# Performance work log

Measured on AMD Instinct MI355X. Metric: run time of the kernel, lower is better.

Reference implementation:

```python
import jax, jax.numpy as jnp
import numpy as np

N_NODES = 20000
N_EDGES = 160000
N_GRAPHS = 500
F_IN = 128
HID = 512
N_CLS = 10
N_LAYERS = 3
BN_EPS = 1e-5
BN_BIAS = 1e-4  # BatchNorm1d weight init to 1, bias to 0.0001


def bn(x):
    # training-mode BatchNorm1d with gamma=1, beta=1e-4 (per module init)
    m = jnp.mean(x, axis=0)
    v = jnp.mean((x - m) ** 2, axis=0)
    return (x - m) * jax.lax.rsqrt(v + BN_EPS) + BN_BIAS


def gcn_norm(row, col, edge_weight, num_nodes):
    # add self loops with weight 1, symmetric deg^-1/2 normalization
    loop = jnp.arange(num_nodes)
    r = jnp.concatenate([row, loop])
    c = jnp.concatenate([col, loop])
    w = jnp.concatenate([edge_weight, jnp.ones((num_nodes,), edge_weight.dtype)])
    deg = jax.ops.segment_sum(w, r, num_segments=num_nodes)
    dis = jnp.where(deg > 0, jax.lax.rsqrt(deg), jnp.zeros_like(deg))
    return r, c, dis[r] * w * dis[c]


def gcn(x, W, b, r, c, norm):
    # x@W then gather source feats, scale by norm, scatter-add to targets
    h = x @ W
    out = jax.ops.segment_sum(norm[:, None] * h[c], r, num_segments=x.shape[0])
    return out + b


def readout(x, W1, b1, W2, b2):
    x = bn(x) @ W1 + b1
    x = jax.nn.relu(x)
    x = bn(x) @ W2 + b2
    return jax.nn.log_softmax(x, axis=-1)


def setup_inputs() -> dict:
    key = jax.random.key(0)
    ks = iter(jax.random.split(key, 40))

    def lin(k, fin, fout):
        return jax.random.normal(k, (fin, fout), jnp.float32) * (1.0 / np.sqrt(fin))

    x = jax.random.normal(next(ks), (N_NODES, F_IN), jnp.float32)
    edge_index = jax.random.randint(next(ks), (2, N_EDGES), 0, N_NODES)
    batch = jnp.sort(jax.random.randint(next(ks), (N_NODES,), 0, N_GRAPHS))
    perm = jax.random.permutation(next(ks), N_GRAPHS)

    inp = {"x": x, "edge_index": edge_index, "batch": batch, "perm": perm}
    inp["conv_feat_W"] = lin(next(ks), F_IN, HID)
    inp["conv_feat_b"] = jnp.zeros((HID,), jnp.float32)
    inp["convs_W"] = jax.random.normal(next(ks), (N_LAYERS, HID, HID), jnp.float32) * (1.0 / np.sqrt(HID))
    inp["convs_b"] = jnp.zeros((N_LAYERS, HID), jnp.float32)
    inp["edge_att_W"] = lin(next(ks), 2 * HID, 2)
    inp["edge_att_b"] = jnp.zeros((2,), jnp.float32)
    inp["node_att_W"] = lin(next(ks), HID, 2)
    inp["node_att_b"] = jnp.zeros((2,), jnp.float32)
    inp["ctx_W"] = lin(next(ks), HID, HID)
    inp["ctx_b"] = jnp.zeros((HID,), jnp.float32)
    inp["obj_W"] = lin(next(ks), HID, HID)
    inp["obj_b"] = jnp.zeros((HID,), jnp.float32)
    for tag in ("c", "o", "co"):
        inp[f"fc1_{tag}_W"] = lin(next(ks), HID, HID)
        inp[f"fc1_{tag}_b"] = jnp.zeros((HID,), jnp.float32)
        inp[f"fc2_{tag}_W"] = lin(next(ks), HID, N_CLS)
        inp[f"fc2_{tag}_b"] = jnp.zeros((N_CLS,), jnp.float32)
    return inp


def reference(x, edge_index, batch, perm,
              conv_feat_W, conv_feat_b, convs_W, convs_b,
              edge_att_W, edge_att_b, node_att_W, node_att_b,
              ctx_W, ctx_b, obj_W, obj_b,
              fc1_c_W, fc1_c_b, fc2_c_W, fc2_c_b,
              fc1_o_W, fc1_o_b, fc2_o_W, fc2_o_b,
              fc1_co_W, fc1_co_b, fc2_co_W, fc2_co_b):
    row, col = edge_index[0], edge_index[1]
    n = x.shape[0]

    x = bn(x)
    x = jax.nn.relu(x @ conv_feat_W + conv_feat_b)  # conv_feat has gfn=True: pure linear

    # unweighted symmetric norm, shared by all stacked convs
    r1, c1, nrm1 = gcn_norm(row, col, jnp.ones((row.shape[0],), x.dtype), n)
    for i in range(N_LAYERS):
        x = bn(x)
        x = jax.nn.relu(gcn(x, convs_W[i], convs_b[i], r1, c1, nrm1))

    edge_rep = jnp.concatenate([x[row], x[col]], axis=-1)        # [E, 2H]
    edge_att = jax.nn.softmax(edge_rep @ edge_att_W + edge_att_b, axis=-1)
    node_att = jax.nn.softmax(x @ node_att_W + node_att_b, axis=-1)

    xc = node_att[:, :1] * x
    xo = node_att[:, 1:] * x

    rc, cc, nc = gcn_norm(row, col, edge_att[:, 0], n)
    ro, co_, no_ = gcn_norm(row, col, edge_att[:, 1], n)
    xc = jax.nn.relu(gcn(bn(xc), ctx_W, ctx_b, rc, cc, nc))
    xo = jax.nn.relu(gcn(bn(xo), obj_W, obj_b, ro, co_, no_))

    xc = jax.ops.segment_sum(xc, batch, num_segments=N_GRAPHS)   # global_add_pool
    xo = jax.ops.segment_sum(xo, batch, num_segments=N_GRAPHS)

    xc_logis = readout(xc, fc1_c_W, fc1_c_b, fc2_c_W, fc2_c_b)
    xo_logis = readout(xo, fc1_o_W, fc1_o_b, fc2_o_W, fc2_o_b)
    # cat_or_add == 'add', with_random shuffle realized by perm
    xco_logis = readout(xc[perm] + xo, fc1_co_W, fc1_co_b, fc2_co_W, fc2_co_b)
    return xc_logis, xo_logis, xco_logis
```

## Files before the change

kernel.cpp:

```cpp
#include <hip/hip_runtime.h>
#include <stdint.h>

#define NN 20000
#define NE 160000
#define NG 500
#define FIN 128
#define HID 512
#define NCLS 10
#define BNG 256
#define NB3 32

typedef __attribute__((ext_vector_type(8))) short short8;
typedef __attribute__((ext_vector_type(4))) float f32x4;
typedef __attribute__((ext_vector_type(4))) unsigned short ushort4v;

__device__ __forceinline__ float bf2f(unsigned int u){
  union{unsigned int i; float f;} x; x.i = u<<16; return x.f;
}
__device__ __forceinline__ unsigned short f2bf(float f){
  union{float f; unsigned int i;} x; x.f=f;
  unsigned int r = x.i + 0x7fffu + ((x.i>>16)&1u);
  return (unsigned short)(r>>16);
}
__device__ __forceinline__ unsigned int pk2(float a, float b){
  return (unsigned int)f2bf(a) | ((unsigned int)f2bf(b) << 16);
}

__device__ __forceinline__ void gload16(unsigned short* lds, const unsigned short* g){
  __builtin_amdgcn_global_load_lds((const __attribute__((address_space(1))) unsigned int*)g,
                                   (__attribute__((address_space(3))) unsigned int*)lds,
                                   16, 0, 0);
}

__device__ __forceinline__ void fma8(float* acc, uint4 v, float w){
  acc[0] += w*bf2f(v.x & 0xffffu); acc[1] += w*bf2f(v.x >> 16);
  acc[2] += w*bf2f(v.y & 0xffffu); acc[3] += w*bf2f(v.y >> 16);
  acc[4] += w*bf2f(v.z & 0xffffu); acc[5] += w*bf2f(v.z >> 16);
  acc[6] += w*bf2f(v.w & 0xffffu); acc[7] += w*bf2f(v.w >> 16);
}

__global__ void sentinel_k(float* out){ out[0] = 12345.0f; }

struct W2BT { const float* src[9]; unsigned short* dst[9]; };
__global__ void setup_all(W2BT p, int* __restrict__ cnt, int* __restrict__ fillc,
                          float* __restrict__ degc, float* __restrict__ dego,
                          float* __restrict__ Sc, float* __restrict__ So,
                          float* __restrict__ stats6){
  int idx = blockIdx.x*blockDim.x + threadIdx.x;
  if (idx < FIN*HID + 8*HID*HID){
    int seg, off, K;
    if (idx < FIN*HID){ seg = 0; off = idx; K = FIN; }
    else {
      int r = idx - FIN*HID;
      seg = 1 + (r >> 18); off = r & (HID*HID-1); K = HID;
    }
    int k = off >> 9, n = off & 511;
    p.dst[seg][(size_t)n*K + k] = f2bf(p.src[seg][off]);
  }
  if (idx < NN){ cnt[idx]=0; fillc[idx]=0; degc[idx]=1.0f; dego[idx]=1.0f; Sc[idx]=0.f; So[idx]=0.f; }
  if (idx < 6*1024) stats6[idx] = 0.f;
}

__global__ __launch_bounds__(1024) void bnstats_p(const float* __restrict__ X, int M, int F,
                                                  float* __restrict__ partials){
  __shared__ float lds[1024*9];
  const int t = threadIdx.x;
  const int cg = F >> 2;
  const int cid = t & (cg-1);
  const int rid = t / cg;
  const int rpb = 1024 / cg;
  float s0=0,s1=0,s2=0,s3=0,q0=0,q1=0,q2=0,q3=0;
  const int rowsPer = (M + BNG - 1)/BNG;
  int r0 = blockIdx.x*rowsPer, r1 = r0 + rowsPer; if (r1 > M) r1 = M;
  for (int r = r0 + rid; r < r1; r += rpb){
    float4 v = *(const float4*)&X[(size_t)r*F + cid*4];
    s0+=v.x; q0+=v.x*v.x; s1+=v.y; q1+=v.y*v.y; s2+=v.z; q2+=v.z*v.z; s3+=v.w; q3+=v.w*v.w;
  }
  int base = (rid*cg + cid)*9;
  lds[base+0]=s0; lds[base+1]=s1; lds[base+2]=s2; lds[base+3]=s3;
  lds[base+4]=q0; lds[base+5]=q1; lds[base+6]=q2; lds[base+7]=q3;
  __syncthreads();
  if (t < cg*8){
    int ci = t >> 3, i = t & 7;
    float acc = 0.f;
    for (int g=0; g<rpb; ++g) acc += lds[(g*cg + ci)*9 + i];
    int col = ci*4 + (i & 3);
    partials[(size_t)blockIdx.x*(2*F) + ((i < 4) ? col : F + col)] = acc;
  }
}

__global__ __launch_bounds__(1024) void bnstats_dual(const unsigned short* __restrict__ X,
                                                     const float* __restrict__ na,
                                                     float* __restrict__ partials){
  __shared__ float lds[1024*17];
  const int t = threadIdx.x;
  const int cid = t & 127;
  const int rid = t >> 7;
  float sC[4]={0,0,0,0}, qC[4]={0,0,0,0}, sO[4]={0,0,0,0}, qO[4]={0,0,0,0};
  const int rowsPer = (NN + BNG - 1)/BNG;
  int r0 = blockIdx.x*rowsPer, r1 = r0 + rowsPer; if (r1 > NN) r1 = NN;
  for (int r = r0 + rid; r < r1; r += 8){
    float a0 = na[2*r], a1 = na[2*r+1];
    uint2 u = *(const uint2*)&X[(size_t)r*HID + cid*4];
    float e[4] = {bf2f(u.x & 0xffffu), bf2f(u.x >> 16), bf2f(u.y & 0xffffu), bf2f(u.y >> 16)};
#pragma unroll
    for (int i=0;i<4;i++){
      float vc = e[i]*a0, vo = e[i]*a1;
      sC[i]+=vc; qC[i]+=vc*vc; sO[i]+=vo; qO[i]+=vo*vo;
    }
  }
  int base = (rid*128 + cid)*17;
#pragma unroll
  for (int i=0;i<4;i++){
    lds[base+i]=sC[i]; lds[base+4+i]=qC[i]; lds[base+8+i]=sO[i]; lds[base+12+i]=qO[i];
  }
  __syncthreads();
  for (int idx = t; idx < 2048; idx += 1024){
    int ci = idx >> 4, i = idx & 15;
    float acc = 0.f;
    for (int g=0; g<8; ++g) acc += lds[(g*128 + ci)*17 + i];
    int grp = i >> 2, col = ci*4 + (i & 3);
    partials[(size_t)blockIdx.x*2048 + grp*HID + col] = acc;
  }
}

__global__ void bnfin_red(const float* __restrict__ partials, int stride, int off,
                          int M, int F, float* __restrict__ mstat){
  __shared__ float lds[4][64][2];
  int t = threadIdx.x;
  int cl = t & 63, ch = t >> 6;
  int c = blockIdx.x*64 + cl;
  float s = 0.f, q = 0.f;
  if (c < F){
    for (int b = ch*64; b < ch*64 + 64; ++b){
      s += partials[(size_t)b*stride + off + c];
      q += partials[(size_t)b*stride + off + F + c];
    }
  }
  lds[ch][cl][0] = s; lds[ch][cl][1] = q;
  __syncthreads();
  if (ch == 0 && c < F){
    s = lds[0][cl][0]+lds[1][cl][0]+lds[2][cl][0]+lds[3][cl][0];
    q = lds[0][cl][1]+lds[1][cl][1]+lds[2][cl][1]+lds[3][cl][1];
    float m = s/(float)M;
    float v = q/(float)M - m*m;
    mstat[c] = m;
    mstat[F+c] = rsqrtf(v + 1e-5f);
  }
}

__global__ void bnfin_red2(const float* __restrict__ partials, float* __restrict__ mstatCO){
  __shared__ float lds[4][64][2];
  int t = threadIdx.x;
  int cl = t & 63, ch = t >> 6;
  int c = blockIdx.x*64 + cl;
  int off = blockIdx.y*1024;
  float s = 0.f, q = 0.f;
  for (int b = ch*64; b < ch*64 + 64; ++b){
    s += partials[(size_t)b*2048 + off + c];
    q += partials[(size_t)b*2048 + off + HID + c];
  }
  lds[ch][cl][0] = s; lds[ch][cl][1] = q;
  __syncthreads();
  if (ch == 0){
    s = lds[0][cl][0]+lds[1][cl][0]+lds[2][cl][0]+lds[3][cl][0];
    q = lds[0][cl][1]+lds[1][cl][1]+lds[2][cl][1]+lds[3][cl][1];
    float m = s/(float)NN;
    float v = q/(float)NN - m*m;
    mstatCO[blockIdx.y*1024 + c] = m;
    mstatCO[blockIdx.y*1024 + HID + c] = rsqrtf(v + 1e-5f);
  }
}

__global__ void bncast(const float* __restrict__ X, const float* __restrict__ mstat,
                       int M, int F, unsigned short* __restrict__ out){
  int idx = blockIdx.x*blockDim.x + threadIdx.x;
  int total4 = M*F/4;
  if (idx >= total4) return;
  int base = idx*4;
  int c = base & (F-1);
  float4 v = *(const float4*)&X[base];
  ushort4v o;
  o[0] = f2bf((v.x - mstat[c+0])*mstat[F+c+0] + 1e-4f);
  o[1] = f2bf((v.y - mstat[c+1])*mstat[F+c+1] + 1e-4f);
  o[2] = f2bf((v.z - mstat[c+2])*mstat[F+c+2] + 1e-4f);
  o[3] = f2bf((v.w - mstat[c+3])*mstat[F+c+3] + 1e-4f);
  *(ushort4v*)&out[base] = o;
}

__global__ void csr_count(const int* __restrict__ ei, int* __restrict__ cnt){
  int e = blockIdx.x*blockDim.x + threadIdx.x;
  if (e < NE) atomicAdd(&cnt[ei[e]], 1);
}

__global__ __launch_bounds__(1024) void scan1(const int* __restrict__ cnt, int* __restrict__ rowp,
                                              float* __restrict__ dis1, int* __restrict__ bsum){
  __shared__ int buf[1024];
  int t = threadIdx.x;
  int i = blockIdx.x*1024 + t;
  int v = 0;
  if (i < NN){ v = cnt[i] + 1; dis1[i] = rsqrtf((float)v); }
  buf[t] = v;
  __syncthreads();
  for (int off=1; off<1024; off<<=1){
    int xv = (t >= off) ? buf[t-off] : 0;
    __syncthreads();
    buf[t] += xv;
    __syncthreads();
  }
  if (i < NN) rowp[i+1] = buf[t];
  if (t == 1023) bsum[blockIdx.x] = buf[1023];
}

__global__ __launch_bounds__(1024) void scan3(int* __restrict__ rowp, const int* __restrict__ bsum){
  __shared__ int base;
  int bx = blockIdx.x;
  if (threadIdx.x == 0){
    int a = 0;
    for (int b=0; b<bx; ++b) a += bsum[b];
    base = a;
  }
  __syncthreads();
  int i = bx*1024 + threadIdx.x;
  if (i < NN) rowp[i+1] += base;
  if (i == 0) rowp[0] = 0;
}

__global__ void csr_fill(const int* __restrict__ ei, const int* __restrict__ rowp,
                         const int* __restrict__ cnt, int* __restrict__ fillc,
                         const float* __restrict__ dis1,
                         int* __restrict__ ccol, int* __restrict__ crow, int* __restrict__ ceid,
                         int2* __restrict__ cw1){
  int id = blockIdx.x*blockDim.x + threadIdx.x;
  if (id < NE){
    int r = ei[id], c = ei[NE + id];
    int pos = atomicAdd(&fillc[r], 1);
    int idx = rowp[r] + pos;
    ccol[idx] = c; crow[idx] = r; ceid[idx] = id;
    cw1[idx] = make_int2(c, __float_as_int(dis1[r]*dis1[c]));
  } else if (id < NE + NN){
    int i = id - NE;
    int idx = rowp[i] + cnt[i];
    ccol[idx] = i; crow[idx] = i; ceid[idx] = -1;
    cw1[idx] = make_int2(i, __float_as_int(dis1[i]*dis1[i]));
  }
}

__global__ void att_node(const unsigned short* __restrict__ X, const float* __restrict__ nW,
                         const float* __restrict__ nb, const float* __restrict__ eW,
                         float* __restrict__ na, float* __restrict__ eab){
  __shared__ float wnl[1024], wet[1024], web[1024];
  int t = threadIdx.x;
  for (int i=t; i<1024; i+=256){ wnl[i]=nW[i]; wet[i]=eW[i]; web[i]=eW[1024+i]; }
  __syncthreads();
  int wv = blockIdx.x*4 + (t >> 6);
  int l = t & 63;
  uint4 u = ((const uint4*)(X + (size_t)wv*HID))[l];
  float xv[8] = {bf2f(u.x&0xffffu), bf2f(u.x>>16), bf2f(u.y&0xffffu), bf2f(u.y>>16),
                 bf2f(u.z&0xffffu), bf2f(u.z>>16), bf2f(u.w&0xffffu), bf2f(u.w>>16)};
  float s0=0,s1=0,s2=0,s3=0,s4=0,s5=0;
#pragma unroll
  for (int j=0; j<8; ++j){
    int k = l*8 + j;
    float x = xv[j];
    s0 += x * wnl[2*k];   s1 += x * wnl[2*k+1];
    s2 += x * wet[2*k];   s3 += x * wet[2*k+1];
    s4 += x * web[2*k];   s5 += x * web[2*k+1];
  }
  for (int m=1; m<64; m<<=1){
    s0 += __shfl_xor(s0,m); s1 += __shfl_xor(s1,m); s2 += __shfl_xor(s2,m);
    s3 += __shfl_xor(s3,m); s4 += __shfl_xor(s4,m); s5 += __shfl_xor(s5,m);
  }
  if (l == 0){
    float z0 = s0 + nb[0], z1 = s1 + nb[1];
    float mx = fmaxf(z0,z1);
    float e0 = expf(z0-mx), e1 = expf(z1-mx);
    float inv = 1.0f/(e0+e1);
    na[2*wv] = e0*inv; na[2*wv+1] = e1*inv;
    eab[4*wv] = s2; eab[4*wv+1] = s3; eab[4*wv+2] = s4; eab[4*wv+3] = s5;
  }
}

__global__ void att_edge(const int* __restrict__ ei, const float* __restrict__ eab,
                         const float* __restrict__ eb, float* __restrict__ att,
                         float* __restrict__ degc, float* __restrict__ dego){
  int e = blockIdx.x*blockDim.x + threadIdx.x;
  if (e >= NE) return;
  int r = ei[e], c = ei[NE+e];
  float z0 = eab[4*r]   + eab[4*c+2] + eb[0];
  float z1 = eab[4*r+1] + eab[4*c+3] + eb[1];
  float mx = fmaxf(z0,z1);
  float e0 = expf(z0-mx), e1 = expf(z1-mx);
  float inv = 1.0f/(e0+e1);
  float a0 = e0*inv, a1 = e1*inv;
  att[2*e] = a0; att[2*e+1] = a1;
  atomicAdd(&degc[r], a0);
  atomicAdd(&dego[r], a1);
}

__global__ void wco_kernel(const int* __restrict__ crow, const int* __restrict__ ccol,
                           const int* __restrict__ ceid, const float* __restrict__ att,
                           const float* __restrict__ degc, const float* __restrict__ dego,
                           const float* __restrict__ na,
                           float* __restrict__ wcv, float* __restrict__ wov,
                           float* __restrict__ Sc, float* __restrict__ So){
  int j = blockIdx.x*blockDim.x + threadIdx.x;
  if (j >= NE + NN) return;
  int r = crow[j], c = ccol[j], e = ceid[j];
  float a0 = (e < 0) ? 1.0f : att[2*e];
  float a1 = (e < 0) ? 1.0f : att[2*e+1];
  float wc = rsqrtf(degc[r]) * a0 * rsqrtf(degc[c]);
  float wo = rsqrtf(dego[r]) * a1 * rsqrtf(dego[c]);
  wcv[j] = wc * na[2*c];
  wov[j] = wo * na[2*c+1];
  atomicAdd(&Sc[r], wc);
  atomicAdd(&So[r], wo);
}

__global__ __launch_bounds__(256) void aggregate_bn(const unsigned short* __restrict__ A,
                                                    const int* __restrict__ rowp,
                                                    const int2* __restrict__ cw,
                                                    const float* __restrict__ stats,
                                                    float invM,
                                                    unsigned short* __restrict__ out){
  int row = blockIdx.x*4 + (threadIdx.x >> 6);
  int l = threadIdx.x & 63;
  const uint4* Av = (const uint4*)A;
  int s = rowp[row], e = rowp[row+1];
  float acc[8] = {0,0,0,0,0,0,0,0};
  float sw = 0.f;
  int j = s;
  for (; j+3 < e; j += 4){
    int2 p0 = cw[j], p1 = cw[j+1], p2 = cw[j+2], p3 = cw[j+3];
    float w0 = __int_as_float(p0.y), w1 = __int_as_float(p1.y);
    float w2 = __int_as_float(p2.y), w3 = __int_as_float(p3.y);
    uint4 v0 = Av[(size_t)p0.x*64 + l];
    uint4 v1 = Av[(size_t)p1.x*64 + l];
    uint4 v2 = Av[(size_t)p2.x*64 + l];
    uint4 v3 = Av[(size_t)p3.x*64 + l];
    fma8(acc, v0, w0); fma8(acc, v1, w1); fma8(acc, v2, w2); fma8(acc, v3, w3);
    sw += w0 + w1 + w2 + w3;
  }
  for (; j < e; ++j){
    int2 p = cw[j];
    float w = __int_as_float(p.y);
    uint4 v = Av[(size_t)p.x*64 + l];
    fma8(acc, v, w);
    sw += w;
  }
  float g[8];
#pragma unroll
  for (int i=0;i<8;i++){
    int c = l*8 + i;
    float m = stats[c]*invM;
    float rs = rsqrtf(stats[512+c]*invM - m*m + 1e-5f);
    g[i] = rs*acc[i] + sw*(1e-4f - m*rs);
  }
  uint4 o;
  o.x = pk2(g[0],g[1]); o.y = pk2(g[2],g[3]); o.z = pk2(g[4],g[5]); o.w = pk2(g[6],g[7]);
  ((uint4*)out)[(size_t)row*64 + l] = o;
}

__global__ __launch_bounds__(256) void aggregate_dual(const unsigned short* __restrict__ A,
                                                      const int* __restrict__ rowp,
                                                      const int* __restrict__ ccol,
                                                      const float* __restrict__ wc,
                                                      const float* __restrict__ wo,
                                                      const float* __restrict__ Sc,
                                                      const float* __restrict__ So,
                                                      const float* __restrict__ mstatCO,
                                                      unsigned short* __restrict__ outC,
                                                      unsigned short* __restrict__ outO){
  int row = blockIdx.x*4 + (threadIdx.x >> 6);
  int l = threadIdx.x & 63;
  const uint4* Av = (const uint4*)A;
  int s = rowp[row], e = rowp[row+1];
  float aC[8] = {0,0,0,0,0,0,0,0};
  float aO[8] = {0,0,0,0,0,0,0,0};
  int j = s;
  for (; j+3 < e; j += 4){
    int c0 = ccol[j], c1 = ccol[j+1], c2 = ccol[j+2], c3 = ccol[j+3];
    float wc0=wc[j], wc1=wc[j+1], wc2=wc[j+2], wc3=wc[j+3];
    float wo0=wo[j], wo1=wo[j+1], wo2=wo[j+2], wo3=wo[j+3];
    uint4 v0 = Av[(size_t)c0*64 + l];
    uint4 v1 = Av[(size_t)c1*64 + l];
    uint4 v2 = Av[(size_t)c2*64 + l];
    uint4 v3 = Av[(size_t)c3*64 + l];
    fma8(aC, v0, wc0); fma8(aO, v0, wo0);
    fma8(aC, v1, wc1); fma8(aO, v1, wo1);
    fma8(aC, v2, wc2); fma8(aO, v2, wo2);
    fma8(aC, v3, wc3); fma8(aO, v3, wo3);
  }
  for (; j < e; ++j){
    uint4 v = Av[(size_t)ccol[j]*64 + l];
    fma8(aC, v, wc[j]); fma8(aO, v, wo[j]);
  }
  float ScR = Sc[row], SoR = So[row];
  float gC[8], gO[8];
#pragma unroll
  for (int i=0;i<8;i++){
    int c = l*8 + i;
    float mc = mstatCO[c],      rc = mstatCO[512+c];
    float mo = mstatCO[1024+c], ro = mstatCO[1536+c];
    gC[i] = rc*aC[i] + ScR*(1e-4f - mc*rc);
    gO[i] = ro*aO[i] + SoR*(1e-4f - mo*ro);
  }
  uint4 oc, oo;
  oc.x = pk2(gC[0],gC[1]); oc.y = pk2(gC[2],gC[3]); oc.z = pk2(gC[4],gC[5]); oc.w = pk2(gC[6],gC[7]);
  oo.x = pk2(gO[0],gO[1]); oo.y = pk2(gO[2],gO[3]); oo.z = pk2(gO[4],gO[5]); oo.w = pk2(gO[6],gO[7]);
  ((uint4*)outC)[(size_t)row*64 + l] = oc;
  ((uint4*)outO)[(size_t)row*64 + l] = oo;
}

__global__ __launch_bounds__(256) void gemm_bt(const unsigned short* __restrict__ A,
                                               const unsigned short* __restrict__ Bt,
                                               unsigned short* __restrict__ O,
                                               const float* __restrict__ bias,
                                               float* __restrict__ stats,
                                               int M, int K, int relu, int split,
                                               const unsigned short* A2,
                                               const unsigned short* Bt2,
                                               unsigned short* O2,
                                               const float* bias2){
  extern __shared__ unsigned short smem[];
  unsigned short* As0 = smem;
  unsigned short* Bs0 = smem + 8192;
  unsigned short* Cs  = smem;
  const int tid = threadIdx.x;
  const int w = tid >> 6, l = tid & 63;

  int lin = blockIdx.x;
  int total = gridDim.x;
  int q = total >> 3, r = total & 7;
  int xcd = lin & 7, idx = lin >> 3;
  int swz = (xcd < r ? xcd*(q+1) : r*(q+1) + (xcd - r)*q) + idx;
  if (split && swz >= split){ A = A2; Bt = Bt2; O = O2; bias = bias2; swz -= split; }
  const int m0 = (swz >> 2)*128, n0 = (swz & 3)*128;

  const int wm = w >> 1, wn = w & 1;
  const int lr = l & 15, lh = l >> 4;

  f32x4 acc[4][4];
#pragma unroll
  for (int i=0;i<4;i++)
#pragma unroll
    for (int j=0;j<4;j++) acc[i][j] = 0.0f;

  const int q0 = w*2, q1 = w*2+1;
  const int sub = l >> 2;
  const int kc  = (l & 3)*8;
  int ma0 = m0 + q0*16 + sub; if (ma0 >= M) ma0 = M-1;
  int ma1 = m0 + q1*16 + sub; if (ma1 >= M) ma1 = M-1;
  const int nb0 = n0 + q0*16 + sub;
  const int nb1 = n0 + q1*16 + sub;
  const unsigned short* Ar0 = A + (size_t)ma0*K + kc;
  const unsigned short* Ar1 = A + (size_t)ma1*K + kc;
  const unsigned short* Br0 = Bt + (size_t)nb0*K + kc;
  const unsigned short* Br1 = Bt + (size_t)nb1*K + kc;

  const int NT = K >> 5;
  gload16(&As0[q0*512], Ar0);
  gload16(&As0[q1*512], Ar1);
  gload16(&Bs0[q0*512], Br0);
  gload16(&Bs0[q1*512], Br1);
  int cur = 0;
  for (int t=0; t<NT; ++t){
    if (t+1 < NT){
      int k1 = (t+1) << 5;
      gload16(&As0[(cur^1)*4096 + q0*512], Ar0 + k1);
      gload16(&As0[(cur^1)*4096 + q1*512], Ar1 + k1);
      gload16(&Bs0[(cur^1)*4096 + q0*512], Br0 + k1);
      gload16(&Bs0[(cur^1)*4096 + q1*512], Br1 + k1);
      asm volatile("s_waitcnt vmcnt(4)" ::: "memory");
    } else {
      asm volatile("s_waitcnt vmcnt(0)" ::: "memory");
    }
    __builtin_amdgcn_s_barrier();
    asm volatile("" ::: "memory");
    short8 af[4], bfr[4];
#pragma unroll
    for (int fm=0; fm<4; ++fm) af[fm]  = *(const short8*)&As0[cur*4096 + (wm*64 + fm*16 + lr)*32 + lh*8];
#pragma unroll
    for (int fn=0; fn<4; ++fn) bfr[fn] = *(const short8*)&Bs0[cur*4096 + (wn*64 + fn*16 + lr)*32 + lh*8];
#pragma unroll
    for (int fm=0; fm<4; ++fm)
#pragma unroll
      for (int fn=0; fn<4; ++fn)
        acc[fm][fn] = __builtin_amdgcn_mfma_f32_16x16x32_bf16(af[fm], bfr[fn], acc[fm][fn], 0, 0, 0);
    asm volatile("" ::: "memory");
    __builtin_amdgcn_s_barrier();
    asm volatile("" ::: "memory");
    cur ^= 1;
  }
  float bv[4], cs[4]={0,0,0,0}, cq[4]={0,0,0,0};
  int col[4];
#pragma unroll
  for (int fn=0; fn<4; ++fn){ col[fn] = n0 + wn*64 + fn*16 + lr; bv[fn] = bias[col[fn]]; }
#pragma unroll
  for (int fm=0; fm<4; ++fm){
#pragma unroll
    for (int j=0; j<4; ++j){
      int trow = wm*64 + fm*16 + lh*4 + j;
      bool valid = (m0 + trow) < M;
#pragma unroll
      for (int fn=0; fn<4; ++fn){
        float v = acc[fm][fn][j] + bv[fn];
        if (relu) v = fmaxf(v, 0.f);
        Cs[trow*136 + wn*64 + fn*16 + lr] = f2bf(v);
        if (valid){ cs[fn] += v; cq[fn] += v*v; }
      }
    }
  }
  __syncthreads();
#pragma unroll
  for (int i=0;i<8;i++){
    int trow = i*16 + (tid>>4);
    int colb = (tid&15)*8;
    uint4 vv = *(const uint4*)&Cs[trow*136 + colb];
    int grow = m0 + trow;
    if (grow < M) *(uint4*)&O[(size_t)grow*HID + n0 + colb] = vv;
  }
  if (stats){
#pragma unroll
    for (int m=16; m<64; m<<=1){
#pragma unroll
      for (int fn=0; fn<4; ++fn){ cs[fn] += __shfl_xor(cs[fn], m); cq[fn] += __shfl_xor(cq[fn], m); }
    }
    if (lh == 0){
#pragma unroll
      for (int fn=0; fn<4; ++fn){
        atomicAdd(&stats[col[fn]], cs[fn]);
        atomicAdd(&stats[512+col[fn]], cq[fn]);
      }
    }
  }
}

struct FC1P { const unsigned short* Bt[3]; const float* bias[3]; };
__global__ __launch_bounds__(256) void gemm_fc1(const unsigned short* __restrict__ A, FC1P p,
                                                unsigned short* __restrict__ O,
                                                float* __restrict__ statsB){
  __shared__ unsigned short As[2][128*32];
  __shared__ unsigned short Bs[2][128*32];
  const int tid = threadIdx.x;
  const int w = tid >> 6, l = tid & 63;
  const int m0 = blockIdx.x*128, n0 = blockIdx.y*128;
  const int branch = blockIdx.x >> 2;
  const unsigned short* Bt = p.Bt[branch];
  const float* bias = p.bias[branch];
  float* stats = statsB + branch*1024;
  const int K = HID;
  const int wm = w >> 1, wn = w & 1;
  const int lr = l & 15, lh = l >> 4;

  f32x4 acc[4][4];
#pragma unroll
  for (int i=0;i<4;i++)
#pragma unroll
    for (int j=0;j<4;j++) acc[i][j] = 0.0f;

  const int q0 = w*2, q1 = w*2+1;
  const int sub = l >> 2;
  const int kc  = (l & 3)*8;
  const int ma0 = m0 + q0*16 + sub;
  const int ma1 = m0 + q1*16 + sub;
  const int nb0 = n0 + q0*16 + sub;
  const int nb1 = n0 + q1*16 + sub;
  const unsigned short* Ar0 = A + (size_t)ma0*K + kc;
  const unsigned short* Ar1 = A + (size_t)ma1*K + kc;
  const unsigned short* Br0 = Bt + (size_t)nb0*K + kc;
  const unsigned short* Br1 = Bt + (size_t)nb1*K + kc;

  const int NT = K >> 5;
  gload16(&As[0][q0*512], Ar0);
  gload16(&As[0][q1*512], Ar1);
  gload16(&Bs[0][q0*512], Br0);
  gload16(&Bs[0][q1*512], Br1);
  int cur = 0;
  for (int t=0; t<NT; ++t){
    if (t+1 < NT){
      int k1 = (t+1) << 5;
      gload16(&As[cur^1][q0*512], Ar0 + k1);
      gload16(&As[cur^1][q1*512], Ar1 + k1);
      gload16(&Bs[cur^1][q0*512], Br0 + k1);
      gload16(&Bs[cur^1][q1*512], Br1 + k1);
      asm volatile("s_waitcnt vmcnt(4)" ::: "memory");
    } else {
      asm volatile("s_waitcnt vmcnt(0)" ::: "memory");
    }
    __builtin_amdgcn_s_barrier();
    asm volatile("" ::: "memory");
    short8 af[4], bfr[4];
#pragma unroll
    for (int fm=0; fm<4; ++fm) af[fm]  = *(const short8*)&As[cur][(wm*64 + fm*16 + lr)*32 + lh*8];
#pragma unroll
    for (int fn=0; fn<4; ++fn) bfr[fn] = *(const short8*)&Bs[cur][(wn*64 + fn*16 + lr)*32 + lh*8];
#pragma unroll
    for (int fm=0; fm<4; ++fm)
#pragma unroll
      for (int fn=0; fn<4; ++fn)
        acc[fm][fn] = __builtin_amdgcn_mfma_f32_16x16x32_bf16(af[fm], bfr[fn], acc[fm][fn], 0, 0, 0);
    asm volatile("" ::: "memory");
    __builtin_amdgcn_s_barrier();
    asm volatile("" ::: "memory");
    cur ^= 1;
  }
  float bv[4], cs[4]={0,0,0,0}, cq[4]={0,0,0,0};
  int col[4];
#pragma unroll
  for (int fn=0; fn<4; ++fn){ col[fn] = n0 + wn*64 + fn*16 + lr; bv[fn] = bias[col[fn]]; }
#pragma unroll
  for (int fm=0; fm<4; ++fm){
#pragma unroll
    for (int j=0; j<4; ++j){
      int row = m0 + wm*64 + fm*16 + lh*4 + j;
      bool real = (row & 511) < NG;
#pragma unroll
      for (int fn=0; fn<4; ++fn){
        float v = fmaxf(acc[fm][fn][j] + bv[fn], 0.f);
        O[(size_t)row*HID + col[fn]] = f2bf(v);
        if (real){ cs[fn] += v; cq[fn] += v*v; }
      }
    }
  }
#pragma unroll
  for (int m=16; m<64; m<<=1){
#pragma unroll
    for (int fn=0; fn<4; ++fn){ cs[fn] += __shfl_xor(cs[fn], m); cq[fn] += __shfl_xor(cq[fn], m); }
  }
  if (lh == 0){
#pragma unroll
    for (int fn=0; fn<4; ++fn){
      atomicAdd(&stats[col[fn]], cs[fn]);
      atomicAdd(&stats[512+col[fn]], cq[fn]);
    }
  }
}

__global__ void pool2(const unsigned short* __restrict__ XC, const unsigned short* __restrict__ XO,
                      const int* __restrict__ batch, float* __restrict__ gc, float* __restrict__ go){
  int g = blockIdx.x;
  int t = threadIdx.x;
  const unsigned short* X = blockIdx.y ? XO : XC;
  float* out = blockIdx.y ? go : gc;
  int lo = 0, hi = NN;
  while (lo < hi){ int mid = (lo+hi) >> 1; if (batch[mid] < g) lo = mid+1; else hi = mid; }
  int s = lo;
  lo = 0; hi = NN;
  while (lo < hi){ int mid = (lo+hi) >> 1; if (batch[mid] < g+1) lo = mid+1; else hi = mid; }
  int e = lo;
  float a0 = 0.f, a1 = 0.f;
  for (int i=s; i<e; ++i){
    unsigned int v = *(const unsigned int*)&X[(size_t)i*HID + t*2];
    a0 += bf2f(v & 0xffffu); a1 += bf2f(v >> 16);
  }
  out[(size_t)g*HID + t*2]     = a0;
  out[(size_t)g*HID + t*2 + 1] = a1;
}

__global__ __launch_bounds__(256) void bnstats3(const float* __restrict__ gc, const float* __restrict__ go,
                                                const int* __restrict__ perm, float* __restrict__ partials){
  __shared__ float lds[256*9];
  int br = blockIdx.y;
  int t = threadIdx.x;
  int cid = t & 127, rid = t >> 7;
  float s[4]={0,0,0,0}, q[4]={0,0,0,0};
  const int rowsPer = (NG + NB3 - 1)/NB3;
  int r0 = blockIdx.x*rowsPer, r1 = r0 + rowsPer; if (r1 > NG) r1 = NG;
  for (int r = r0 + rid; r < r1; r += 2){
    float4 v;
    if (br == 0)      v = *(const float4*)&gc[(size_t)r*HID + cid*4];
    else if (br == 1) v = *(const float4*)&go[(size_t)r*HID + cid*4];
    else {
      int ps = perm[r];
      float4 a = *(const float4*)&gc[(size_t)ps*HID + cid*4];
      float4 b = *(const float4*)&go[(size_t)r*HID + cid*4];
      v = make_float4(a.x+b.x, a.y+b.y, a.z+b.z, a.w+b.w);
    }
    float e[4] = {v.x, v.y, v.z, v.w};
#pragma unroll
    for (int i=0;i<4;i++){ s[i]+=e[i]; q[i]+=e[i]*e[i]; }
  }
  int base = (rid*128 + cid)*9;
#pragma unroll
  for (int i=0;i<4;i++){ lds[base+i]=s[i]; lds[base+4+i]=q[i]; }
  __syncthreads();
  for (int o = t; o < 1024; o += 256){
    int issq = o >> 9, col = o & 511;
    int ci = col >> 2, i = col & 3;
    float acc = lds[(0*128 + ci)*9 + issq*4 + i] + lds[(1*128 + ci)*9 + issq*4 + i];
    partials[(size_t)(br*NB3 + blockIdx.x)*1024 + issq*512 + col] = acc;
  }
}

__global__ void bnfin3(const float* __restrict__ partials, float* __restrict__ mstat3){
  __shared__ float lds[4][64][2];
  int t = threadIdx.x;
  int cl = t & 63, ch = t >> 6;
  int c = blockIdx.x*64 + cl;
  int br = blockIdx.y;
  float s = 0.f, q = 0.f;
  for (int b = ch*8; b < ch*8 + 8; ++b){
    s += partials[(size_t)(br*NB3 + b)*1024 + c];
    q += partials[(size_t)(br*NB3 + b)*1024 + 512 + c];
  }
  lds[ch][cl][0] = s; lds[ch][cl][1] = q;
  __syncthreads();
  if (ch == 0){
    s = lds[0][cl][0]+lds[1][cl][0]+lds[2][cl][0]+lds[3][cl][0];
    q = lds[0][cl][1]+lds[1][cl][1]+lds[2][cl][1]+lds[3][cl][1];
    float m = s/(float)NG;
    float v = q/(float)NG - m*m;
    mstat3[br*1024 + c] = m;
    mstat3[br*1024 + 512 + c] = rsqrtf(v + 1e-5f);
  }
}

__global__ void bncast3(const float* __restrict__ gc, const float* __restrict__ go,
                        const int* __restrict__ perm, const float* __restrict__ mstat3,
                        unsigned short* __restrict__ out){
  int idx = blockIdx.x*blockDim.x + threadIdx.x;
  if (idx >= 1536*128) return;
  int r = idx >> 7;
  int cg = idx & 127;
  int br = r >> 9, lr = r & 511;
  ushort4v o;
  if (lr >= NG){ o[0]=0; o[1]=0; o[2]=0; o[3]=0; }
  else {
    float4 v;
    if (br == 0)      v = *(const float4*)&gc[(size_t)lr*HID + cg*4];
    else if (br == 1) v = *(const float4*)&go[(size_t)lr*HID + cg*4];
    else {
      int ps = perm[lr];
      float4 a = *(const float4*)&gc[(size_t)ps*HID + cg*4];
      float4 b = *(const float4*)&go[(size_t)lr*HID + cg*4];
      v = make_float4(a.x+b.x, a.y+b.y, a.z+b.z, a.w+b.w);
    }
    const float* ms = mstat3 + br*1024;
    int c = cg*4;
    o[0] = f2bf((v.x - ms[c+0])*ms[512+c+0] + 1e-4f);
    o[1] = f2bf((v.y - ms[c+1])*ms[512+c+1] + 1e-4f);
    o[2] = f2bf((v.z - ms[c+2])*ms[512+c+2] + 1e-4f);
    o[3] = f2bf((v.w - ms[c+3])*ms[512+c+3] + 1e-4f);
  }
  *(ushort4v*)&out[(size_t)r*HID + cg*4] = o;
}

struct ROP { const float* W2[3]; const float* b2[3]; };
__global__ void readout_final3(const unsigned short* __restrict__ T, const float* __restrict__ statsB,
                               float invM, ROP p, float* __restrict__ out){
  int g = blockIdx.x;
  int br = blockIdx.y;
  int l = threadIdx.x;
  const float* stats = statsB + br*1024;
  const float* W2 = p.W2[br];
  const float* b2 = p.b2[br];
  float acc[NCLS];
#pragma unroll
  for (int c=0; c<NCLS; ++c) acc[c] = 0.f;
  uint4 u = ((const uint4*)(T + (size_t)(br*512 + g)*HID))[l];
  float xv[8] = {bf2f(u.x&0xffffu), bf2f(u.x>>16), bf2f(u.y&0xffffu), bf2f(u.y>>16),
                 bf2f(u.z&0xffffu), bf2f(u.z>>16), bf2f(u.w&0xffffu), bf2f(u.w>>16)};
#pragma unroll
  for (int j=0; j<8; ++j){
    int k = l*8 + j;
    float m = stats[k]*invM;
    float rs = rsqrtf(stats[512+k]*invM - m*m + 1e-5f);
    float v = (xv[j] - m)*rs + 1e-4f;
#pragma unroll
    for (int c=0; c<NCLS; ++c) acc[c] += v * W2[k*NCLS + c];
  }
  for (int m=1; m<64; m<<=1){
#pragma unroll
    for (int c=0; c<NCLS; ++c) acc[c] += __shfl_xor(acc[c], m);
  }
  if (l == 0){
    float z[NCLS];
    float mx = -1e30f;
#pragma unroll
    for (int c=0; c<NCLS; ++c){ z[c] = acc[c] + b2[c]; mx = fmaxf(mx, z[c]); }
    float s = 0.f;
#pragma unroll
    for (int c=0; c<NCLS; ++c) s += expf(z[c]-mx);
    float lse = mx + logf(s);
#pragma unroll
    for (int c=0; c<NCLS; ++c) out[(size_t)(br*NG + g)*NCLS + c] = z[c] - lse;
  }
}

extern "C" void kernel_launch(void* const* d_in, const int* in_sizes, int n_in,
                              void* d_out, int out_size, void* d_ws, size_t ws_size,
                              hipStream_t stream){
  (void)in_sizes; (void)n_in; (void)out_size;
  const float* x      = (const float*)d_in[0];
  const int*   ei     = (const int*)d_in[1];
  const int*   batch  = (const int*)d_in[2];
  const int*   perm   = (const int*)d_in[3];
  const float* convfW = (const float*)d_in[4];
  const float* convfB = (const float*)d_in[5];
  const float* convsW = (const float*)d_in[6];
  const float* convsB = (const float*)d_in[7];
  const float* eattW  = (const float*)d_in[8];
  const float* eattB  = (const float*)d_in[9];
  const float* nattW  = (const float*)d_in[10];
  const float* nattB  = (const float*)d_in[11];
  const float* ctxW   = (const float*)d_in[12];
  const float* ctxB   = (const float*)d_in[13];
  const float* objW   = (const float*)d_in[14];
  const float* objB   = (const float*)d_in[15];
  const float* fc1W[3] = {(const float*)d_in[16], (const float*)d_in[20], (const float*)d_in[24]};
  const float* fc1B[3] = {(const float*)d_in[17], (const float*)d_in[21], (const float*)d_in[25]};
  const float* fc2W[3] = {(const float*)d_in[18], (const float*)d_in[22], (const float*)d_in[26]};
  const float* fc2B[3] = {(const float*)d_in[19], (const float*)d_in[23], (const float*)d_in[27]};
  float* out = (float*)d_out;

  char* p = (char*)d_ws;
  auto alloc = [&](size_t bytes)->char*{ char* r = p; p += (bytes + 255) & ~((size_t)255); return r; };
  const int T = NE + NN;
  unsigned short* Xbf = (unsigned short*)alloc((size_t)NN*HID*2);
  unsigned short* Gbf = (unsigned short*)alloc((size_t)NN*HID*2);
  unsigned short* GbfO= (unsigned short*)alloc((size_t)NN*HID*2);
  unsigned short* XbfO= (unsigned short*)alloc((size_t)NN*HID*2);
  unsigned short* Abf = (unsigned short*)alloc((size_t)NN*FIN*2);
  unsigned short* WtF = (unsigned short*)alloc((size_t)HID*FIN*2);
  unsigned short* WtL = (unsigned short*)alloc((size_t)3*HID*HID*2);
  unsigned short* WtC = (unsigned short*)alloc((size_t)HID*HID*2);
  unsigned short* WtO = (unsigned short*)alloc((size_t)HID*HID*2);
  unsigned short* WtR = (unsigned short*)alloc((size_t)3*HID*HID*2);
  int* cnt   = (int*)alloc((size_t)NN*4);
  int* fillc = (int*)alloc((size_t)NN*4);
  int* rowp  = (int*)alloc((size_t)(NN+1)*4);
  int* bsum  = (int*)alloc(32*4);
  int* ccol  = (int*)alloc((size_t)T*4);
  int* crow  = (int*)alloc((size_t)T*4);
  int* ceid  = (int*)alloc((size_t)T*4);
  int2* cw1  = (int2*)alloc((size_t)T*8);
  float* wcv = (float*)alloc((size_t)T*4);
  float* wov = (float*)alloc((size_t)T*4);
  float* dis1 = (float*)alloc((size_t)NN*4);
  float* degc = (float*)alloc((size_t)NN*4);
  float* dego = (float*)alloc((size_t)NN*4);
  float* Sc   = (float*)alloc((size_t)NN*4);
  float* So   = (float*)alloc((size_t)NN*4);
  float* stats6 = (float*)alloc(6*1024*4);
  float* mstat  = (float*)alloc(2*HID*4);
  float* mstatCO= (float*)alloc(2*1024*4);
  float* mstat3 = (float*)alloc(3*1024*4);
  float* na   = (float*)alloc((size_t)NN*2*4);
  float* eab  = (float*)alloc((size_t)NN*4*4);
  float* att  = (float*)alloc((size_t)NE*2*4);
  float* gc   = (float*)alloc((size_t)NG*HID*4);
  float* go   = (float*)alloc((size_t)NG*HID*4);
  float* part = (float*)alloc((size_t)BNG*2048*4);
  if ((size_t)(p - (char*)d_ws) > ws_size){
    sentinel_k<<<1,1,0,stream>>>(out);
    return;
  }
  unsigned short* Abf3 = Abf;
  unsigned short* Gbf3 = GbfO;
  const float invNN = 1.0f/(float)NN;
  const float invNG = 1.0f/(float)NG;
  const int GEMM_LDS = 128*136*2;

  W2BT wp;
  wp.src[0]=convfW; wp.dst[0]=WtF;
  for (int i=0;i<3;i++){ wp.src[1+i]=convsW+(size_t)i*HID*HID; wp.dst[1+i]=WtL+(size_t)i*HID*HID; }
  wp.src[4]=ctxW; wp.dst[4]=WtC;
  wp.src[5]=objW; wp.dst[5]=WtO;
  for (int i=0;i<3;i++){ wp.src[6+i]=fc1W[i]; wp.dst[6+i]=WtR+(size_t)i*HID*HID; }
  setup_all<<<(FIN*HID + 8*HID*HID + 255)/256, 256, 0, stream>>>(wp, cnt, fillc, degc, dego, Sc, So, stats6);

  csr_count<<<(NE+255)/256,256,0,stream>>>(ei, cnt);
  scan1<<<(NN+1023)/1024,1024,0,stream>>>(cnt, rowp, dis1, bsum);
  scan3<<<(NN+1023)/1024,1024,0,stream>>>(rowp, bsum);
  csr_fill<<<(T+255)/256,256,0,stream>>>(ei, rowp, cnt, fillc, dis1, ccol, crow, ceid, cw1);

  const int NBLK = ((NN+127)/128)*4;

  bnstats_p<<<BNG,1024,0,stream>>>(x, NN, FIN, part);
  bnfin_red<<<(FIN+63)/64,256,0,stream>>>(part, 2*FIN, 0, NN, FIN, mstat);
  bncast<<<((NN*FIN/4)+255)/256,256,0,stream>>>(x, mstat, NN, FIN, Abf);
  gemm_bt<<<NBLK,256,GEMM_LDS,stream>>>(Abf, WtF, Xbf, convfB, stats6, NN, FIN, 1,
                                        0, nullptr, nullptr, nullptr, nullptr);

  for (int i=0;i<3;i++){
    aggregate_bn<<<NN/4,256,0,stream>>>(Xbf, rowp, cw1, stats6 + i*1024, invNN, Gbf);
    gemm_bt<<<NBLK,256,GEMM_LDS,stream>>>(Gbf, WtL+(size_t)i*HID*HID, Xbf,
                                          convsB+(size_t)i*HID,
                                          (i<2) ? (stats6 + (i+1)*1024) : nullptr,
                                          NN, HID, 1, 0, nullptr, nullptr, nullptr, nullptr);
  }

  att_node<<<NN/4,256,0,stream>>>(Xbf, nattW, nattB, eattW, na, eab);
  att_edge<<<(NE+255)/256,256,0,stream>>>(ei, eab, eattB, att, degc, dego);
  wco_kernel<<<(T+255)/256,256,0,stream>>>(crow, ccol, ceid, att, degc, dego, na, wcv, wov, Sc, So);

  bnstats_dual<<<BNG,1024,0,stream>>>(Xbf, na, part);
  bnfin_red2<<<dim3(8,2),256,0,stream>>>(part, mstatCO);
  aggregate_dual<<<NN/4,256,0,stream>>>(Xbf, rowp, ccol, wcv, wov, Sc, So, mstatCO, Gbf, GbfO);
  gemm_bt<<<2*NBLK,256,GEMM_LDS,stream>>>(Gbf, WtC, Xbf, ctxB, nullptr, NN, HID, 1,
                                          NBLK, GbfO, WtO, XbfO, objB);
  pool2<<<dim3(NG,2),256,0,stream>>>(Xbf, XbfO, batch, gc, go);

  bnstats3<<<dim3(NB3,3),256,0,stream>>>(gc, go, perm, part);
  bnfin3<<<dim3(8,3),256,0,stream>>>(part, mstat3);
  bncast3<<<(1536*128+255)/256,256,0,stream>>>(gc, go, perm, mstat3, Abf3);
  FC1P fp;
  for (int i=0;i<3;i++){ fp.Bt[i] = WtR+(size_t)i*HID*HID; fp.bias[i] = fc1B[i]; }
  gemm_fc1<<<dim3(12,4),256,0,stream>>>(Abf3, fp, Gbf3, stats6 + 3*1024);
  ROP rp;
  for (int i=0;i<3;i++){ rp.W2[i] = fc2W[i]; rp.b2[i] = fc2B[i]; }
  readout_final3<<<dim3(NG,3),64,0,stream>>>(Gbf3, stats6 + 3*1024, invNG, rp, out);
}
```

Before: 442.6 us.

## Fuse setup kernels, triple-buffer GEMM loads, deepen aggregation unroll, merge readout BN stats

Merges the CSR count, scan and initial BN stats/cast kernels into three combined launches that split work by block index. The same is done for the readout BN stats, which now use a single-pass kernel per branch. Both GEMMs move from double to triple buffering with a two-tile prefetch distance and a larger dynamic LDS allocation. The aggregation kernels unroll neighbor gathers by eight to keep more loads in flight. The goal is fewer launch and serialization gaps and better latency hiding, at the cost of more LDS per GEMM block (which may lower occupancy) and higher register pressure.

```diff
diff --git a/kernel.cpp b/kernel.cpp
--- a/kernel.cpp
+++ b/kernel.cpp
@@ -8,7 +8,6 @@
 #define HID 512
 #define NCLS 10
 #define BNG 256
-#define NB3 32
 
 typedef __attribute__((ext_vector_type(8))) short short8;
 typedef __attribute__((ext_vector_type(4))) float f32x4;
@@ -61,19 +60,24 @@
   if (idx < 6*1024) stats6[idx] = 0.f;
 }
 
-__global__ __launch_bounds__(1024) void bnstats_p(const float* __restrict__ X, int M, int F,
-                                                  float* __restrict__ partials){
+__global__ __launch_bounds__(1024) void d1_count_stats(const int* __restrict__ ei, int* __restrict__ cnt,
+                                                       const float* __restrict__ X, float* __restrict__ partials){
   __shared__ float lds[1024*9];
   const int t = threadIdx.x;
-  const int cg = F >> 2;
+  if (blockIdx.x >= BNG){
+    int e = (blockIdx.x - BNG)*1024 + t;
+    if (e < NE) atomicAdd(&cnt[ei[e]], 1);
+    return;
+  }
+  const int cg = FIN >> 2;
   const int cid = t & (cg-1);
   const int rid = t / cg;
   const int rpb = 1024 / cg;
   float s0=0,s1=0,s2=0,s3=0,q0=0,q1=0,q2=0,q3=0;
-  const int rowsPer = (M + BNG - 1)/BNG;
-  int r0 = blockIdx.x*rowsPer, r1 = r0 + rowsPer; if (r1 > M) r1 = M;
+  const int rowsPer = (NN + BNG - 1)/BNG;
+  int r0 = blockIdx.x*rowsPer, r1 = r0 + rowsPer; if (r1 > NN) r1 = NN;
   for (int r = r0 + rid; r < r1; r += rpb){
-    float4 v = *(const float4*)&X[(size_t)r*F + cid*4];
+    float4 v = *(const float4*)&X[(size_t)r*FIN + cid*4];
     s0+=v.x; q0+=v.x*v.x; s1+=v.y; q1+=v.y*v.y; s2+=v.z; q2+=v.z*v.z; s3+=v.w; q3+=v.w*v.w;
   }
   int base = (rid*cg + cid)*9;
@@ -85,80 +89,39 @@
     float acc = 0.f;
     for (int g=0; g<rpb; ++g) acc += lds[(g*cg + ci)*9 + i];
     int col = ci*4 + (i & 3);
-    partials[(size_t)blockIdx.x*(2*F) + ((i < 4) ? col : F + col)] = acc;
-  }
-}
-
-__global__ __launch_bounds__(1024) void bnstats_dual(const unsigned short* __restrict__ X,
-                                                     const float* __restrict__ na,
-                                                     float* __restrict__ partials){
-  __shared__ float lds[1024*17];
-  const int t = threadIdx.x;
-  const int cid = t & 127;
-  const int rid = t >> 7;
-  float sC[4]={0,0,0,0}, qC[4]={0,0,0,0}, sO[4]={0,0,0,0}, qO[4]={0,0,0,0};
-  const int rowsPer = (NN + BNG - 1)/BNG;
-  int r0 = blockIdx.x*rowsPer, r1 = r0 + rowsPer; if (r1 > NN) r1 = NN;
-  for (int r = r0 + rid; r < r1; r += 8){
-    float a0 = na[2*r], a1 = na[2*r+1];
-    uint2 u = *(const uint2*)&X[(size_t)r*HID + cid*4];
-    float e[4] = {bf2f(u.x & 0xffffu), bf2f(u.x >> 16), bf2f(u.y & 0xffffu), bf2f(u.y >> 16)};
-#pragma unroll
-    for (int i=0;i<4;i++){
-      float vc = e[i]*a0, vo = e[i]*a1;
-      sC[i]+=vc; qC[i]+=vc*vc; sO[i]+=vo; qO[i]+=vo*vo;
-    }
-  }
-  int base = (rid*128 + cid)*17;
-#pragma unroll
-  for (int i=0;i<4;i++){
-    lds[base+i]=sC[i]; lds[base+4+i]=qC[i]; lds[base+8+i]=sO[i]; lds[base+12+i]=qO[i];
-  }
-  __syncthreads();
-  for (int idx = t; idx < 2048; idx += 1024){
-    int ci = idx >> 4, i = idx & 15;
-    float acc = 0.f;
-    for (int g=0; g<8; ++g) acc += lds[(g*128 + ci)*17 + i];
-    int grp = i >> 2, col = ci*4 + (i & 3);
-    partials[(size_t)blockIdx.x*2048 + grp*HID + col] = acc;
-  }
-}
-
-__global__ void bnfin_red(const float* __restrict__ partials, int stride, int off,
-                          int M, int F, float* __restrict__ mstat){
+    partials[(size_t)blockIdx.x*(2*FIN) + ((i < 4) ? col : FIN + col)] = acc;
+  }
+}
+
+__global__ __launch_bounds__(1024) void d2_scan_fin(const int* __restrict__ cnt, int* __restrict__ rowp,
+                                                    float* __restrict__ dis1, int* __restrict__ bsum,
+                                                    const float* __restrict__ partials, float* __restrict__ mstat){
+  __shared__ int buf[1024];
   __shared__ float lds[4][64][2];
   int t = threadIdx.x;
+  if (blockIdx.x < 20){
+    int i = blockIdx.x*1024 + t;
+    int v = 0;
+    if (i < NN){ v = cnt[i] + 1; dis1[i] = rsqrtf((float)v); }
+    buf[t] = v;
+    __syncthreads();
+    for (int off=1; off<1024; off<<=1){
+      int xv = (t >= off) ? buf[t-off] : 0;
+      __syncthreads();
+      buf[t] += xv;
+      __syncthreads();
+    }
+    if (i < NN) rowp[i+1] = buf[t];
+    if (t == 1023) bsum[blockIdx.x] = buf[1023];
+    return;
+  }
+  if (t >= 256) return;
   int cl = t & 63, ch = t >> 6;
-  int c = blockIdx.x*64 + cl;
-  float s = 0.f, q = 0.f;
-  if (c < F){
-    for (int b = ch*64; b < ch*64 + 64; ++b){
-      s += partials[(size_t)b*stride + off + c];
-      q += partials[(size_t)b*stride + off + F + c];
-    }
-  }
-  lds[ch][cl][0] = s; lds[ch][cl][1] = q;
-  __syncthreads();
-  if (ch == 0 && c < F){
-    s = lds[0][cl][0]+lds[1][cl][0]+lds[2][cl][0]+lds[3][cl][0];
-    q = lds[0][cl][1]+lds[1][cl][1]+lds[2][cl][1]+lds[3][cl][1];
-    float m = s/(float)M;
-    float v = q/(float)M - m*m;
-    mstat[c] = m;
-    mstat[F+c] = rsqrtf(v + 1e-5f);
-  }
-}
-
-__global__ void bnfin_red2(const float* __restrict__ partials, float* __restrict__ mstatCO){
-  __shared__ float lds[4][64][2];
-  int t = threadIdx.x;
-  int cl = t & 63, ch = t >> 6;
-  int c = blockIdx.x*64 + cl;
-  int off = blockIdx.y*1024;
+  int c = (blockIdx.x - 20)*64 + cl;
   float s = 0.f, q = 0.f;
   for (int b = ch*64; b < ch*64 + 64; ++b){
-    s += partials[(size_t)b*2048 + off + c];
-    q += partials[(size_t)b*2048 + off + HID + c];
+    s += partials[(size_t)b*(2*FIN) + c];
+    q += partials[(size_t)b*(2*FIN) + FIN + c];
   }
   lds[ch][cl][0] = s; lds[ch][cl][1] = q;
   __syncthreads();
@@ -167,63 +130,41 @@
     q = lds[0][cl][1]+lds[1][cl][1]+lds[2][cl][1]+lds[3][cl][1];
     float m = s/(float)NN;
     float v = q/(float)NN - m*m;
-    mstatCO[blockIdx.y*1024 + c] = m;
-    mstatCO[blockIdx.y*1024 + HID + c] = rsqrtf(v + 1e-5f);
-  }
-}
-
-__global__ void bncast(const float* __restrict__ X, const float* __restrict__ mstat,
-                       int M, int F, unsigned short* __restrict__ out){
-  int idx = blockIdx.x*blockDim.x + threadIdx.x;
-  int total4 = M*F/4;
+    mstat[c] = m;
+    mstat[FIN+c] = rsqrtf(v + 1e-5f);
+  }
+}
+
+__global__ __launch_bounds__(1024) void d3_scan_cast(int* __restrict__ rowp, const int* __restrict__ bsum,
+                                                     const float* __restrict__ X, const float* __restrict__ mstat,
+                                                     unsigned short* __restrict__ out){
+  __shared__ int base;
+  int t = threadIdx.x;
+  if (blockIdx.x < 20){
+    int bx = blockIdx.x;
+    if (t == 0){
+      int a = 0;
+      for (int b=0; b<bx; ++b) a += bsum[b];
+      base = a;
+    }
+    __syncthreads();
+    int i = bx*1024 + t;
+    if (i < NN) rowp[i+1] += base;
+    if (i == 0) rowp[0] = 0;
+    return;
+  }
+  int idx = (blockIdx.x - 20)*1024 + t;
+  int total4 = NN*FIN/4;
   if (idx >= total4) return;
-  int base = idx*4;
-  int c = base & (F-1);
-  float4 v = *(const float4*)&X[base];
+  int b4 = idx*4;
+  int c = b4 & (FIN-1);
+  float4 v = *(const float4*)&X[b4];
   ushort4v o;
-  o[0] = f2bf((v.x - mstat[c+0])*mstat[F+c+0] + 1e-4f);
-  o[1] = f2bf((v.y - mstat[c+1])*mstat[F+c+1] + 1e-4f);
-  o[2] = f2bf((v.z - mstat[c+2])*mstat[F+c+2] + 1e-4f);
-  o[3] = f2bf((v.w - mstat[c+3])*mstat[F+c+3] + 1e-4f);
-  *(ushort4v*)&out[base] = o;
-}
-
-__global__ void csr_count(const int* __restrict__ ei, int* __restrict__ cnt){
-  int e = blockIdx.x*blockDim.x + threadIdx.x;
-  if (e < NE) atomicAdd(&cnt[ei[e]], 1);
-}
-
-__global__ __launch_bounds__(1024) void scan1(const int* __restrict__ cnt, int* __restrict__ rowp,
-                                              float* __restrict__ dis1, int* __restrict__ bsum){
-  __shared__ int buf[1024];
-  int t = threadIdx.x;
-  int i = blockIdx.x*1024 + t;
-  int v = 0;
-  if (i < NN){ v = cnt[i] + 1; dis1[i] = rsqrtf((float)v); }
-  buf[t] = v;
-  __syncthreads();
-  for (int off=1; off<1024; off<<=1){
-    int xv = (t >= off) ? buf[t-off] : 0;
-    __syncthreads();
-    buf[t] += xv;
-    __syncthreads();
-  }
-  if (i < NN) rowp[i+1] = buf[t];
-  if (t == 1023) bsum[blockIdx.x] = buf[1023];
-}
-
-__global__ __launch_bounds__(1024) void scan3(int* __restrict__ rowp, const int* __restrict__ bsum){
-  __shared__ int base;
-  int bx = blockIdx.x;
-  if (threadIdx.x == 0){
-    int a = 0;
-    for (int b=0; b<bx; ++b) a += bsum[b];
-    base = a;
-  }
-  __syncthreads();
-  int i = bx*1024 + threadIdx.x;
-  if (i < NN) rowp[i+1] += base;
-  if (i == 0) rowp[0] = 0;
+  o[0] = f2bf((v.x - mstat[c+0])*mstat[FIN+c+0] + 1e-4f);
+  o[1] = f2bf((v.y - mstat[c+1])*mstat[FIN+c+1] + 1e-4f);
+  o[2] = f2bf((v.z - mstat[c+2])*mstat[FIN+c+2] + 1e-4f);
+  o[3] = f2bf((v.w - mstat[c+3])*mstat[FIN+c+3] + 1e-4f);
+  *(ushort4v*)&out[b4] = o;
 }
 
 __global__ void csr_fill(const int* __restrict__ ei, const int* __restrict__ rowp,
@@ -246,6 +187,64 @@
   }
 }
 
+__global__ __launch_bounds__(1024) void bnstats_dual(const unsigned short* __restrict__ X,
+                                                     const float* __restrict__ na,
+                                                     float* __restrict__ partials){
+  __shared__ float lds[1024*17];
+  const int t = threadIdx.x;
+  const int cid = t & 127;
+  const int rid = t >> 7;
+  float sC[4]={0,0,0,0}, qC[4]={0,0,0,0}, sO[4]={0,0,0,0}, qO[4]={0,0,0,0};
+  const int rowsPer = (NN + BNG - 1)/BNG;
+  int r0 = blockIdx.x*rowsPer, r1 = r0 + rowsPer; if (r1 > NN) r1 = NN;
+  for (int r = r0 + rid; r < r1; r += 8){
+    float a0 = na[2*r], a1 = na[2*r+1];
+    uint2 u = *(const uint2*)&X[(size_t)r*HID + cid*4];
+    float e[4] = {bf2f(u.x & 0xffffu), bf2f(u.x >> 16), bf2f(u.y & 0xffffu), bf2f(u.y >> 16)};
+#pragma unroll
+    for (int i=0;i<4;i++){
+      float vc = e[i]*a0, vo = e[i]*a1;
+      sC[i]+=vc; qC[i]+=vc*vc; sO[i]+=vo; qO[i]+=vo*vo;
+    }
+  }
+  int base = (rid*128 + cid)*17;
+#pragma unroll
+  for (int i=0;i<4;i++){
+    lds[base+i]=sC[i]; lds[base+4+i]=qC[i]; lds[base+8+i]=sO[i]; lds[base+12+i]=qO[i];
+  }
+  __syncthreads();
+  for (int idx = t; idx < 2048; idx += 1024){
+    int ci = idx >> 4, i = idx & 15;
+    float acc = 0.f;
+    for (int g=0; g<8; ++g) acc += lds[(g*128 + ci)*17 + i];
+    int grp = i >> 2, col = ci*4 + (i & 3);
+    partials[(size_t)blockIdx.x*2048 + grp*HID + col] = acc;
+  }
+}
+
+__global__ void bnfin_red2(const float* __restrict__ partials, float* __restrict__ mstatCO){
+  __shared__ float lds[4][64][2];
+  int t = threadIdx.x;
+  int cl = t & 63, ch = t >> 6;
+  int c = blockIdx.x*64 + cl;
+  int off = blockIdx.y*1024;
+  float s = 0.f, q = 0.f;
+  for (int b = ch*64; b < ch*64 + 64; ++b){
+    s += partials[(size_t)b*2048 + off + c];
+    q += partials[(size_t)b*2048 + off + HID + c];
+  }
+  lds[ch][cl][0] = s; lds[ch][cl][1] = q;
+  __syncthreads();
+  if (ch == 0){
+    s = lds[0][cl][0]+lds[1][cl][0]+lds[2][cl][0]+lds[3][cl][0];
+    q = lds[0][cl][1]+lds[1][cl][1]+lds[2][cl][1]+lds[3][cl][1];
+    float m = s/(float)NN;
+    float v = q/(float)NN - m*m;
+    mstatCO[blockIdx.y*1024 + c] = m;
+    mstatCO[blockIdx.y*1024 + HID + c] = rsqrtf(v + 1e-5f);
+  }
+}
+
 __global__ void att_node(const unsigned short* __restrict__ X, const float* __restrict__ nW,
                          const float* __restrict__ nb, const float* __restrict__ eW,
                          float* __restrict__ na, float* __restrict__ eab){
@@ -330,16 +329,23 @@
   float acc[8] = {0,0,0,0,0,0,0,0};
   float sw = 0.f;
   int j = s;
+  for (; j+7 < e; j += 8){
+    int2 p[8]; uint4 v[8];
+#pragma unroll
+    for (int k=0;k<8;k++) p[k] = cw[j+k];
+#pragma unroll
+    for (int k=0;k<8;k++) v[k] = Av[(size_t)p[k].x*64 + l];
+#pragma unroll
+    for (int k=0;k<8;k++){ float w = __int_as_float(p[k].y); fma8(acc, v[k], w); sw += w; }
+  }
   for (; j+3 < e; j += 4){
-    int2 p0 = cw[j], p1 = cw[j+1], p2 = cw[j+2], p3 = cw[j+3];
-    float w0 = __int_as_float(p0.y), w1 = __int_as_float(p1.y);
-    float w2 = __int_as_float(p2.y), w3 = __int_as_float(p3.y);
-    uint4 v0 = Av[(size_t)p0.x*64 + l];
-    uint4 v1 = Av[(size_t)p1.x*64 + l];
-    uint4 v2 = Av[(size_t)p2.x*64 + l];
-    uint4 v3 = Av[(size_t)p3.x*64 + l];
-    fma8(acc, v0, w0); fma8(acc, v1, w1); fma8(acc, v2, w2); fma8(acc, v3, w3);
-    sw += w0 + w1 + w2 + w3;
+    int2 p[4]; uint4 v[4];
+#pragma unroll
+    for (int k=0;k<4;k++) p[k] = cw[j+k];
+#pragma unroll
+    for (int k=0;k<4;k++) v[k] = Av[(size_t)p[k].x*64 + l];
+#pragma unroll
+    for (int k=0;k<4;k++){ float w = __int_as_float(p[k].y); fma8(acc, v[k], w); sw += w; }
   }
   for (; j < e; ++j){
     int2 p = cw[j];
@@ -378,18 +384,23 @@
   float aC[8] = {0,0,0,0,0,0,0,0};
   float aO[8] = {0,0,0,0,0,0,0,0};
   int j = s;
+  for (; j+7 < e; j += 8){
+    int cc[8]; uint4 v[8];
+#pragma unroll
+    for (int k=0;k<8;k++) cc[k] = ccol[j+k];
+#pragma unroll
+    for (int k=0;k<8;k++) v[k] = Av[(size_t)cc[k]*64 + l];
+#pragma unroll
+    for (int k=0;k<8;k++){ fma8(aC, v[k], wc[j+k]); fma8(aO, v[k], wo[j+k]); }
+  }
   for (; j+3 < e; j += 4){
-    int c0 = ccol[j], c1 = ccol[j+1], c2 = ccol[j+2], c3 = ccol[j+3];
-    float wc0=wc[j], wc1=wc[j+1], wc2=wc[j+2], wc3=wc[j+3];
-    float wo0=wo[j], wo1=wo[j+1], wo2=wo[j+2], wo3=wo[j+3];
-    uint4 v0 = Av[(size_t)c0*64 + l];
-    uint4 v1 = Av[(size_t)c1*64 + l];
-    uint4 v2 = Av[(size_t)c2*64 + l];
-    uint4 v3 = Av[(size_t)c3*64 + l];
-    fma8(aC, v0, wc0); fma8(aO, v0, wo0);
-    fma8(aC, v1, wc1); fma8(aO, v1, wo1);
-    fma8(aC, v2, wc2); fma8(aO, v2, wo2);
-    fma8(aC, v3, wc3); fma8(aO, v3, wo3);
+    int cc[4]; uint4 v[4];
+#pragma unroll
+    for (int k=0;k<4;k++) cc[k] = ccol[j+k];
+#pragma unroll
+    for (int k=0;k<4;k++) v[k] = Av[(size_t)cc[k]*64 + l];
+#pragma unroll
+    for (int k=0;k<4;k++){ fma8(aC, v[k], wc[j+k]); fma8(aO, v[k], wo[j+k]); }
   }
   for (; j < e; ++j){
     uint4 v = Av[(size_t)ccol[j]*64 + l];
@@ -423,9 +434,7 @@
                                                unsigned short* O2,
                                                const float* bias2){
   extern __shared__ unsigned short smem[];
-  unsigned short* As0 = smem;
-  unsigned short* Bs0 = smem + 8192;
-  unsigned short* Cs  = smem;
+  unsigned short* Cs = smem;
   const int tid = threadIdx.x;
   const int w = tid >> 6, l = tid & 63;
 
@@ -459,18 +468,27 @@
   const unsigned short* Br1 = Bt + (size_t)nb1*K + kc;
 
   const int NT = K >> 5;
-  gload16(&As0[q0*512], Ar0);
-  gload16(&As0[q1*512], Ar1);
-  gload16(&Bs0[q0*512], Br0);
-  gload16(&Bs0[q1*512], Br1);
+  gload16(&smem[0*8192 + q0*512], Ar0);
+  gload16(&smem[0*8192 + q1*512], Ar1);
+  gload16(&smem[0*8192 + 4096 + q0*512], Br0);
+  gload16(&smem[0*8192 + 4096 + q1*512], Br1);
+  if (NT > 1){
+    gload16(&smem[1*8192 + q0*512], Ar0 + 32);
+    gload16(&smem[1*8192 + q1*512], Ar1 + 32);
+    gload16(&smem[1*8192 + 4096 + q0*512], Br0 + 32);
+    gload16(&smem[1*8192 + 4096 + q1*512], Br1 + 32);
+  }
   int cur = 0;
   for (int t=0; t<NT; ++t){
-    if (t+1 < NT){
-      int k1 = (t+1) << 5;
-      gload16(&As0[(cur^1)*4096 + q0*512], Ar0 + k1);
-      gload16(&As0[(cur^1)*4096 + q1*512], Ar1 + k1);
-      gload16(&Bs0[(cur^1)*4096 + q0*512], Br0 + k1);
-      gload16(&Bs0[(cur^1)*4096 + q1*512], Br1 + k1);
+    if (t+2 < NT){
+      int k1 = (t+2) << 5;
+      int nb = cur + 2; if (nb >= 3) nb -= 3;
+      gload16(&smem[nb*8192 + q0*512], Ar0 + k1);
+      gload16(&smem[nb*8192 + q1*512], Ar1 + k1);
+      gload16(&smem[nb*8192 + 4096 + q0*512], Br0 + k1);
+      gload16(&smem[nb*8192 + 4096 + q1*512], Br1 + k1);
+      asm volatile("s_waitcnt vmcnt(8)" ::: "memory");
+    } else if (t+1 < NT){
       asm volatile("s_waitcnt vmcnt(4)" ::: "memory");
     } else {
       asm volatile("s_waitcnt vmcnt(0)" ::: "memory");
@@ -479,9 +497,9 @@
     asm volatile("" ::: "memory");
     short8 af[4], bfr[4];
 #pragma unroll
-    for (int fm=0; fm<4; ++fm) af[fm]  = *(const short8*)&As0[cur*4096 + (wm*64 + fm*16 + lr)*32 + lh*8];
-#pragma unroll
-    for (int fn=0; fn<4; ++fn) bfr[fn] = *(const short8*)&Bs0[cur*4096 + (wn*64 + fn*16 + lr)*32 + lh*8];
+    for (int fm=0; fm<4; ++fm) af[fm]  = *(const short8*)&smem[cur*8192 + (wm*64 + fm*16 + lr)*32 + lh*8];
+#pragma unroll
+    for (int fn=0; fn<4; ++fn) bfr[fn] = *(const short8*)&smem[cur*8192 + 4096 + (wn*64 + fn*16 + lr)*32 + lh*8];
 #pragma unroll
     for (int fm=0; fm<4; ++fm)
 #pragma unroll
@@ -490,12 +508,17 @@
     asm volatile("" ::: "memory");
     __builtin_amdgcn_s_barrier();
     asm volatile("" ::: "memory");
-    cur ^= 1;
-  }
+    cur += 1; if (cur >= 3) cur = 0;
+  }
+  int dep = __float_as_int(acc[0][0][0]);
+  int z_;
+  asm volatile("v_and_b32 %0, 0, %1" : "=v"(z_) : "v"(dep));
+  const float* biasp = bias + z_;
+
   float bv[4], cs[4]={0,0,0,0}, cq[4]={0,0,0,0};
   int col[4];
 #pragma unroll
-  for (int fn=0; fn<4; ++fn){ col[fn] = n0 + wn*64 + fn*16 + lr; bv[fn] = bias[col[fn]]; }
+  for (int fn=0; fn<4; ++fn){ col[fn] = n0 + wn*64 + fn*16 + lr; bv[fn] = biasp[col[fn]]; }
 #pragma unroll
   for (int fm=0; fm<4; ++fm){
 #pragma unroll
@@ -540,8 +563,7 @@
 __global__ __launch_bounds__(256) void gemm_fc1(const unsigned short* __restrict__ A, FC1P p,
                                                 unsigned short* __restrict__ O,
                                                 float* __restrict__ statsB){
-  __shared__ unsigned short As[2][128*32];
-  __shared__ unsigned short Bs[2][128*32];
+  extern __shared__ unsigned short smem[];
   const int tid = threadIdx.x;
   const int w = tid >> 6, l = tid & 63;
   const int m0 = blockIdx.x*128, n0 = blockIdx.y*128;
@@ -572,18 +594,25 @@
   const unsigned short* Br1 = Bt + (size_t)nb1*K + kc;
 
   const int NT = K >> 5;
-  gload16(&As[0][q0*512], Ar0);
-  gload16(&As[0][q1*512], Ar1);
-  gload16(&Bs[0][q0*512], Br0);
-  gload16(&Bs[0][q1*512], Br1);
+  gload16(&smem[0*8192 + q0*512], Ar0);
+  gload16(&smem[0*8192 + q1*512], Ar1);
+  gload16(&smem[0*8192 + 4096 + q0*512], Br0);
+  gload16(&smem[0*8192 + 4096 + q1*512], Br1);
+  gload16(&smem[1*8192 + q0*512], Ar0 + 32);
+  gload16(&smem[1*8192 + q1*512], Ar1 + 32);
+  gload16(&smem[1*8192 + 4096 + q0*512], Br0 + 32);
+  gload16(&smem[1*8192 + 4096 + q1*512], Br1 + 32);
   int cur = 0;
   for (int t=0; t<NT; ++t){
-    if (t+1 < NT){
-      int k1 = (t+1) << 5;
-      gload16(&As[cur^1][q0*512], Ar0 + k1);
-      gload16(&As[cur^1][q1*512], Ar1 + k1);
-      gload16(&Bs[cur^1][q0*512], Br0 + k1);
-      gload16(&Bs[cur^1][q1*512], Br1 + k1);
+    if (t+2 < NT){
+      int k1 = (t+2) << 5;
+      int nb = cur + 2; if (nb >= 3) nb -= 3;
+      gload16(&smem[nb*8192 + q0*512], Ar0 + k1);
+      gload16(&smem[nb*8192 + q1*512], Ar1 + k1);
+      gload16(&smem[nb*8192 + 4096 + q0*512], Br0 + k1);
+      gload16(&smem[nb*8192 + 4096 + q1*512], Br1 + k1);
+      asm volatile("s_waitcnt vmcnt(8)" ::: "memory");
+    } else if (t+1 < NT){
       asm volatile("s_waitcnt vmcnt(4)" ::: "memory");
     } else {
       asm volatile("s_waitcnt vmcnt(0)" ::: "memory");
@@ -592,9 +621,9 @@
     asm volatile("" ::: "memory");
     short8 af[4], bfr[4];
 #pragma unroll
-    for (int fm=0; fm<4; ++fm) af[fm]  = *(const short8*)&As[cur][(wm*64 + fm*16 + lr)*32 + lh*8];
-#pragma unroll
-    for (int fn=0; fn<4; ++fn) bfr[fn] = *(const short8*)&Bs[cur][(wn*64 + fn*16 + lr)*32 + lh*8];
+    for (int fm=0; fm<4; ++fm) af[fm]  = *(const short8*)&smem[cur*8192 + (wm*64 + fm*16 + lr)*32 + lh*8];
+#pragma unroll
+    for (int fn=0; fn<4; ++fn) bfr[fn] = *(const short8*)&smem[cur*8192 + 4096 + (wn*64 + fn*16 + lr)*32 + lh*8];
 #pragma unroll
     for (int fm=0; fm<4; ++fm)
 #pragma unroll
@@ -603,12 +632,17 @@
     asm volatile("" ::: "memory");
     __builtin_amdgcn_s_barrier();
     asm volatile("" ::: "memory");
-    cur ^= 1;
-  }
+    cur += 1; if (cur >= 3) cur = 0;
+  }
+  int dep = __float_as_int(acc[0][0][0]);
+  int z_;
+  asm volatile("v_and_b32 %0, 0, %1" : "=v"(z_) : "v"(dep));
+  const float* biasp = bias + z_;
+
   float bv[4], cs[4]={0,0,0,0}, cq[4]={0,0,0,0};
   int col[4];
 #pragma unroll
-  for (int fn=0; fn<4; ++fn){ col[fn] = n0 + wn*64 + fn*16 + lr; bv[fn] = bias[col[fn]]; }
+  for (int fn=0; fn<4; ++fn){ col[fn] = n0 + wn*64 + fn*16 + lr; bv[fn] = biasp[col[fn]]; }
 #pragma unroll
   for (int fm=0; fm<4; ++fm){
 #pragma unroll
@@ -658,16 +692,15 @@
   out[(size_t)g*HID + t*2 + 1] = a1;
 }
 
-__global__ __launch_bounds__(256) void bnstats3(const float* __restrict__ gc, const float* __restrict__ go,
-                                                const int* __restrict__ perm, float* __restrict__ partials){
-  __shared__ float lds[256*9];
-  int br = blockIdx.y;
+__global__ __launch_bounds__(1024) void bnstats3f(const float* __restrict__ gc, const float* __restrict__ go,
+                                                  const int* __restrict__ perm, float* __restrict__ mstat3){
+  __shared__ float lds[8*128*9];
+  __shared__ float colsum[512], colsq[512];
+  int br = blockIdx.x;
   int t = threadIdx.x;
   int cid = t & 127, rid = t >> 7;
   float s[4]={0,0,0,0}, q[4]={0,0,0,0};
-  const int rowsPer = (NG + NB3 - 1)/NB3;
-  int r0 = blockIdx.x*rowsPer, r1 = r0 + rowsPer; if (r1 > NG) r1 = NG;
-  for (int r = r0 + rid; r < r1; r += 2){
+  for (int r = rid; r < NG; r += 8){
     float4 v;
     if (br == 0)      v = *(const float4*)&gc[(size_t)r*HID + cid*4];
     else if (br == 1) v = *(const float4*)&go[(size_t)r*HID + cid*4];
@@ -685,34 +718,19 @@
 #pragma unroll
   for (int i=0;i<4;i++){ lds[base+i]=s[i]; lds[base+4+i]=q[i]; }
   __syncthreads();
-  for (int o = t; o < 1024; o += 256){
-    int issq = o >> 9, col = o & 511;
-    int ci = col >> 2, i = col & 3;
-    float acc = lds[(0*128 + ci)*9 + issq*4 + i] + lds[(1*128 + ci)*9 + issq*4 + i];
-    partials[(size_t)(br*NB3 + blockIdx.x)*1024 + issq*512 + col] = acc;
-  }
-}
-
-__global__ void bnfin3(const float* __restrict__ partials, float* __restrict__ mstat3){
-  __shared__ float lds[4][64][2];
-  int t = threadIdx.x;
-  int cl = t & 63, ch = t >> 6;
-  int c = blockIdx.x*64 + cl;
-  int br = blockIdx.y;
-  float s = 0.f, q = 0.f;
-  for (int b = ch*8; b < ch*8 + 8; ++b){
-    s += partials[(size_t)(br*NB3 + b)*1024 + c];
-    q += partials[(size_t)(br*NB3 + b)*1024 + 512 + c];
-  }
-  lds[ch][cl][0] = s; lds[ch][cl][1] = q;
+  {
+    int ci = t >> 3, i = t & 7;
+    float a = 0.f;
+    for (int g=0; g<8; ++g) a += lds[(g*128 + ci)*9 + i];
+    int col = ci*4 + (i & 3);
+    if (i < 4) colsum[col] = a; else colsq[col] = a;
+  }
   __syncthreads();
-  if (ch == 0){
-    s = lds[0][cl][0]+lds[1][cl][0]+lds[2][cl][0]+lds[3][cl][0];
-    q = lds[0][cl][1]+lds[1][cl][1]+lds[2][cl][1]+lds[3][cl][1];
-    float m = s/(float)NG;
-    float v = q/(float)NG - m*m;
-    mstat3[br*1024 + c] = m;
-    mstat3[br*1024 + 512 + c] = rsqrtf(v + 1e-5f);
+  if (t < 512){
+    float m = colsum[t]/(float)NG;
+    float v = colsq[t]/(float)NG - m*m;
+    mstat3[br*1024 + t] = m;
+    mstat3[br*1024 + 512 + t] = rsqrtf(v + 1e-5f);
   }
 }
 
@@ -860,7 +878,7 @@
   unsigned short* Gbf3 = GbfO;
   const float invNN = 1.0f/(float)NN;
   const float invNG = 1.0f/(float)NG;
-  const int GEMM_LDS = 128*136*2;
+  const int GEMM_LDS = 3*8192*2;
 
   W2BT wp;
   wp.src[0]=convfW; wp.dst[0]=WtF;
@@ -870,16 +888,13 @@
   for (int i=0;i<3;i++){ wp.src[6+i]=fc1W[i]; wp.dst[6+i]=WtR+(size_t)i*HID*HID; }
   setup_all<<<(FIN*HID + 8*HID*HID + 255)/256, 256, 0, stream>>>(wp, cnt, fillc, degc, dego, Sc, So, stats6);
 
-  csr_count<<<(NE+255)/256,256,0,stream>>>(ei, cnt);
-  scan1<<<(NN+1023)/1024,1024,0,stream>>>(cnt, rowp, dis1, bsum);
-  scan3<<<(NN+1023)/1024,1024,0,stream>>>(rowp, bsum);
+  d1_count_stats<<<BNG + (NE+1023)/1024, 1024, 0, stream>>>(ei, cnt, x, part);
+  d2_scan_fin<<<20 + FIN/64, 1024, 0, stream>>>(cnt, rowp, dis1, bsum, part, mstat);
+  d3_scan_cast<<<20 + (NN*FIN/4 + 1023)/1024, 1024, 0, stream>>>(rowp, bsum, x, mstat, Abf);
   csr_fill<<<(T+255)/256,256,0,stream>>>(ei, rowp, cnt, fillc, dis1, ccol, crow, ceid, cw1);
 
   const int NBLK = ((NN+127)/128)*4;
 
-  bnstats_p<<<BNG,1024,0,stream>>>(x, NN, FIN, part);
-  bnfin_red<<<(FIN+63)/64,256,0,stream>>>(part, 2*FIN, 0, NN, FIN, mstat);
-  bncast<<<((NN*FIN/4)+255)/256,256,0,stream>>>(x, mstat, NN, FIN, Abf);
   gemm_bt<<<NBLK,256,GEMM_LDS,stream>>>(Abf, WtF, Xbf, convfB, stats6, NN, FIN, 1,
                                         0, nullptr, nullptr, nullptr, nullptr);
 
@@ -902,12 +917,11 @@
                                           NBLK, GbfO, WtO, XbfO, objB);
   pool2<<<dim3(NG,2),256,0,stream>>>(Xbf, XbfO, batch, gc, go);
 
-  bnstats3<<<dim3(NB3,3),256,0,stream>>>(gc, go, perm, part);
-  bnfin3<<<dim3(8,3),256,0,stream>>>(part, mstat3);
+  bnstats3f<<<3,1024,0,stream>>>(gc, go, perm, mstat3);
   bncast3<<<(1536*128+255)/256,256,0,stream>>>(gc, go, perm, mstat3, Abf3);
   FC1P fp;
   for (int i=0;i<3;i++){ fp.Bt[i] = WtR+(size_t)i*HID*HID; fp.bias[i] = fc1B[i]; }
-  gemm_fc1<<<dim3(12,4),256,0,stream>>>(Abf3, fp, Gbf3, stats6 + 3*1024);
+  gemm_fc1<<<dim3(12,4),256,GEMM_LDS,stream>>>(Abf3, fp, Gbf3, stats6 + 3*1024);
   ROP rp;
   for (int i=0;i<3;i++){ rp.W2[i] = fc2W[i]; rp.b2[i] = fc2B[i]; }
   readout_final3<<<dim3(NG,3),64,0,stream>>>(Gbf3, stats6 + 3*1024, invNG, rp, out);
```

Result: slower. 469.3 us (+6.0%).
